# Optimization experiments

Measured on AMD Instinct MI355X. Metric: run time of the kernel, lower is better.

The kernel has to match this reference:

```python
import jax, jax.numpy as jnp
import numpy as np

B, D_IN, D_OUT, N_CTRL = 8192, 512, 512, 8

def setup_inputs() -> dict:
    key = jax.random.key(0)
    k1, k2, k3, k4 = jax.random.split(key, 4)
    inputs = jax.random.normal(k1, (B, D_IN), dtype=jnp.float32)
    # routing weights: positive soft blend coefficients, normalized per sample
    raw = jax.random.uniform(k2, (B, N_CTRL), dtype=jnp.float32)
    weights = raw / jnp.sum(raw, axis=-1, keepdims=True)
    w = jax.random.normal(k3, (N_CTRL, D_IN, D_OUT), dtype=jnp.float32) * 0.05
    b = jax.random.normal(k4, (N_CTRL, D_OUT), dtype=jnp.float32) * 0.05
    return {"inputs": inputs, "weights": weights, "w": w, "b": b}

def reference(inputs, weights, w, b):
    # Original math: w_p = einsum('ji,imk->jmk', weights, w)  [B, D_IN, D_OUT]
    #                out = squeeze(inputs[:, None, :] @ w_p) + weights @ b
    # Fused equivalent avoiding the [B, D_IN, D_OUT] intermediate:
    # run all n_control expert matmuls, then blend by routing weights.
    per_expert = jnp.einsum('bi,cio->cbo', inputs, w)       # [C, B, D_OUT]
    out = jnp.einsum('bc,cbo->bo', weights, per_expert)     # [B, D_OUT]
    out = out + weights @ b                                 # blended bias [B, D_OUT]
    return out
```

## Files before the change

### kernel.cpp

```cpp
#include <hip/hip_runtime.h>

#define B_   8192
#define DIN  512
#define DOUT 512
#define NC   8
#define NCD  (NC * DIN)
#define KSPL 4

typedef float  f32x4 __attribute__((ext_vector_type(4)));
typedef short  s16x8 __attribute__((ext_vector_type(8)));
typedef unsigned short u16x4 __attribute__((ext_vector_type(4)));
typedef unsigned int   u32x4 __attribute__((ext_vector_type(4)));

__device__ __forceinline__ unsigned short f2bf(float f) {
  unsigned u = __builtin_bit_cast(unsigned, f);
  u += 0x7fffu + ((u >> 16) & 1u);
  return (unsigned short)(u >> 16);
}
__device__ __forceinline__ float bf2f(unsigned short h) {
  unsigned u = ((unsigned)h) << 16;
  return __builtin_bit_cast(float, u);
}
__device__ __forceinline__ unsigned cvtpk(float lo, float hi) {
  unsigned r;
  asm("v_cvt_pk_bf16_f32 %0, %1, %2" : "=v"(r) : "v"(lo), "v"(hi));
  return r;
}

__global__ void pack_xw_k(const f32x4* __restrict__ x, u16x4* __restrict__ xb,
                          const float* __restrict__ w, unsigned short* __restrict__ WtF) {
  __shared__ float tile[64][65];
  const int tid = threadIdx.x;
  if (blockIdx.x < 4096) {
    int gid = blockIdx.x * 256 + tid;
    f32x4 v = x[gid];
    u16x4 o;
    o[0] = f2bf(v[0]); o[1] = f2bf(v[1]); o[2] = f2bf(v[2]); o[3] = f2bf(v[3]);
    xb[gid] = o;
    return;
  }
  const int idx = blockIdx.x - 4096;
  const int kb = idx & 63, nb = idx >> 6;
  const int e = kb >> 3, ktl = kb & 7;
#pragma unroll
  for (int it = 0; it < 16; ++it) {
    int u = it * 256 + tid;
    int r = u >> 6, cc = u & 63;
    tile[r][cc] = w[(size_t)(e * 512 + ktl * 64 + r) * DOUT + nb * 64 + cc];
  }
  __syncthreads();
#pragma unroll
  for (int it = 0; it < 2; ++it) {
    int c = it * 256 + tid;
    int n16l = c >> 7, kk = (c >> 6) & 1, l = c & 63;
    int l15 = l & 15, lhi = l >> 4;
    int col_in = n16l * 16 + l15;
    int k_in   = kk * 32 + lhi * 8;
    int n16    = nb * 4 + n16l;
    u16x4 o0, o1;
    o0[0] = f2bf(tile[k_in + 0][col_in]); o0[1] = f2bf(tile[k_in + 1][col_in]);
    o0[2] = f2bf(tile[k_in + 2][col_in]); o0[3] = f2bf(tile[k_in + 3][col_in]);
    o1[0] = f2bf(tile[k_in + 4][col_in]); o1[1] = f2bf(tile[k_in + 5][col_in]);
    o1[2] = f2bf(tile[k_in + 6][col_in]); o1[3] = f2bf(tile[k_in + 7][col_in]);
    size_t base = ((((size_t)e * 32 + n16) * 8 + ktl) * 2 + kk) * 512 + l * 8;
    *(u16x4*)(WtF + base)     = o0;
    *(u16x4*)(WtF + base + 4) = o1;
  }
}

__global__ __launch_bounds__(512, 2) void gemm_k(
    const unsigned short* __restrict__ xb,
    const unsigned short* __restrict__ WtF,
    const float* __restrict__ wt,
    unsigned short* __restrict__ part) {
  extern __shared__ char smem[];
  const int tid  = threadIdx.x;
  const int lane = tid & 63, wid = tid >> 6;
  const int wm = wid >> 2, wn = wid & 3;
  const int l15 = lane & 15, lhi = lane >> 4;

  const int n0   = blockIdx.x;
  const int by   = n0 >> 3;
  const int bx   = (n0 >> 2) & 1;
  const int ks   = n0 & 3;
  const int brow = by * 256, bcol = bx * 256;

  const int srow = tid >> 3, schunk = tid & 7;
  const int swz  = schunk ^ (srow & 7);
  const unsigned short* gA = xb + (size_t)(brow + srow) * DIN + schunk * 8;
  const int adst_off = srow * 128 + swz * 16;

  const unsigned short* bn0 = WtF + (size_t)(ks * 2) * 262144
                                  + (size_t)(bx * 16 + wn * 4 + 0) * 8192 + lane * 8;
  const unsigned short* bn1 = bn0 + 8192;
  const unsigned short* bn2 = bn0 + 16384;
  const unsigned short* bn3 = bn0 + 24576;

  const float* wtp = wt + (size_t)(brow + srow) * NC + ks * 2;
  const float wtv0_0 = wtp[0],            wtv1_0 = wtp[1];
  const float wtv0_1 = wtp[64 * NC],      wtv1_1 = wtp[64 * NC + 1];
  const float wtv0_2 = wtp[128 * NC],     wtv1_2 = wtp[128 * NC + 1];
  const float wtv0_3 = wtp[192 * NC],     wtv1_3 = wtp[192 * NC + 1];

  f32x4 acc[8][4] = {};
  s16x8 areg0, areg1, areg2, areg3;
  s16x8 a[8], b0q[4], b1q[4];
  const int x7    = l15 & 7;
  const int pc0   = (lhi ^ x7) * 16;
  const int pc1   = ((4 + lhi) ^ x7) * 16;
  const int abase = (wm * 128 + l15) * 128;

#define LOAD_B(BQ, et, ktl, kk) {                                            \
    const size_t o_ = (size_t)(et) * 262144 + ((ktl) * 2 + (kk)) * 512;      \
    BQ[0] = *(const s16x8*)(bn0 + o_);                                       \
    BQ[1] = *(const s16x8*)(bn1 + o_);                                       \
    BQ[2] = *(const s16x8*)(bn2 + o_);                                       \
    BQ[3] = *(const s16x8*)(bn3 + o_); }
#define LOAD_AREGS(kt) {                                                     \
    const unsigned short* s_ = gA + ((kt) & 7) * 64;                         \
    areg0 = *(const s16x8*)(s_);                                             \
    areg1 = *(const s16x8*)(s_ + (size_t) 64 * DIN);                         \
    areg2 = *(const s16x8*)(s_ + (size_t)128 * DIN);                         \
    areg3 = *(const s16x8*)(s_ + (size_t)192 * DIN); }
#define SCALE_STORE(AR, S, P, slotb) {                                       \
    u32x4 v_;                                                                \
    v_[0] = cvtpk(bf2f((unsigned short)AR[0]) * (S),                         \
                  bf2f((unsigned short)AR[1]) * (S));                        \
    v_[1] = cvtpk(bf2f((unsigned short)AR[2]) * (S),                         \
                  bf2f((unsigned short)AR[3]) * (S));                        \
    v_[2] = cvtpk(bf2f((unsigned short)AR[4]) * (S),                         \
                  bf2f((unsigned short)AR[5]) * (S));                        \
    v_[3] = cvtpk(bf2f((unsigned short)AR[6]) * (S),                         \
                  bf2f((unsigned short)AR[7]) * (S));                        \
    *(u32x4*)(smem + (slotb) + adst_off + (P) * 8192) = v_; }
#define SCALE_WRITE_ALL(e_, slotb) {                                         \
    SCALE_STORE(areg0, (e_) ? wtv1_0 : wtv0_0, 0, slotb);                    \
    SCALE_STORE(areg1, (e_) ? wtv1_1 : wtv0_1, 1, slotb);                    \
    SCALE_STORE(areg2, (e_) ? wtv1_2 : wtv0_2, 2, slotb);                    \
    SCALE_STORE(areg3, (e_) ? wtv1_3 : wtv0_3, 3, slotb); }
#define RD_A8(slotb, PC) {                                                   \
    const char* pa_ = smem + (slotb) + abase + (PC);                         \
    _Pragma("unroll") for (int m = 0; m < 8; ++m)                            \
      a[m] = *(const s16x8*)(pa_ + m * 2048); }
#define MFMA_HALF(BQ)                                                        \
    _Pragma("unroll") for (int m = 0; m < 8; ++m)                            \
      _Pragma("unroll") for (int n = 0; n < 4; ++n)                          \
        acc[m][n] = __builtin_amdgcn_mfma_f32_16x16x32_bf16(                 \
            a[m], BQ[n], acc[m][n], 0, 0, 0);
#define BAR()   __builtin_amdgcn_s_barrier()
#define PRIO1() __builtin_amdgcn_s_setprio(1)
#define PRIO0() __builtin_amdgcn_s_setprio(0)
#define SBAR0() __builtin_amdgcn_sched_barrier(0)
#define WAITL() asm volatile("s_waitcnt lgkmcnt(0)" ::: "memory")

  LOAD_AREGS(0);
  SCALE_WRITE_ALL(0, 0);
  LOAD_AREGS(1);
  LOAD_B(b0q, 0, 0, 0);
  WAITL();
  BAR();

  for (int t = 0; t < 16; ++t) {
    const int ct = (t & 1) * 32768, ot = 32768 - ct;
    const int ktl = t & 7, et = t >> 3;
    RD_A8(ct, pc0);
    LOAD_B(b1q, et, ktl, 1);
    WAITL(); SBAR0();
    PRIO1(); MFMA_HALF(b0q); PRIO0();
    RD_A8(ct, pc1);
    if (t < 15) {
      SCALE_WRITE_ALL(((t + 1) >> 3), ot);
      if (t < 14) LOAD_AREGS(t + 2);
    }
    WAITL(); SBAR0();
    PRIO1(); MFMA_HALF(b1q); PRIO0();
    if (t < 15) LOAD_B(b0q, ((t + 1) >> 3), ((t + 1) & 7), 0);
    BAR();
  }

  __syncthreads();
  unsigned short* Cs = (unsigned short*)smem;
#pragma unroll
  for (int m = 0; m < 8; ++m)
#pragma unroll
    for (int n = 0; n < 4; ++n) {
      const int row = wm * 128 + m * 16 + lhi * 4;
      const int col = wn * 64 + n * 16 + l15;
      f32x4 v = acc[m][n];
#pragma unroll
      for (int j = 0; j < 4; ++j)
        Cs[(row + j) * 264 + col] = f2bf(v[j]);
    }
  __syncthreads();
  unsigned short* pc = part + (size_t)ks * (B_ * DOUT) + (size_t)brow * DOUT + bcol;
#pragma unroll
  for (int it = 0; it < 16; ++it) {
    const int u = it * 512 + tid;
    const int row = u >> 5, cu = (u & 31) * 8;
    f32x4 v = *(const f32x4*)(Cs + row * 264 + cu);
    *(f32x4*)(pc + (size_t)row * DOUT + cu) = v;
  }
#undef LOAD_B
#undef LOAD_AREGS
#undef SCALE_STORE
#undef SCALE_WRITE_ALL
#undef RD_A8
#undef MFMA_HALF
#undef BAR
#undef PRIO1
#undef PRIO0
#undef SBAR0
#undef WAITL
}

__global__ void reduce_k(const unsigned short* __restrict__ part,
                         const float* __restrict__ wt,
                         const float* __restrict__ bias,
                         float* __restrict__ out) {
  int gid = blockIdx.x * 256 + threadIdx.x;
  int b = gid >> 7;
  int o4 = (gid & 127) << 2;
  float w8[8];
  *(f32x4*)w8       = *(const f32x4*)(wt + (size_t)b * NC);
  *(f32x4*)(w8 + 4) = *(const f32x4*)(wt + (size_t)b * NC + 4);
  f32x4 acc = {0.f, 0.f, 0.f, 0.f};
  const size_t off = (size_t)b * DOUT + o4;
#pragma unroll
  for (int s = 0; s < KSPL; ++s) {
    u16x4 p = *(const u16x4*)(part + (size_t)s * (B_ * DOUT) + off);
#pragma unroll
    for (int i = 0; i < 4; ++i) acc[i] += bf2f(p[i]);
  }
#pragma unroll
  for (int cc = 0; cc < NC; ++cc) {
    f32x4 bi = *(const f32x4*)(bias + cc * DOUT + o4);
#pragma unroll
    for (int i = 0; i < 4; ++i) acc[i] += w8[cc] * bi[i];
  }
  *(f32x4*)(out + off) = acc;
}

__global__ void bias_only_k(const float* __restrict__ wt,
                            const float* __restrict__ bias,
                            float* __restrict__ out) {
  int gid = blockIdx.x * 256 + threadIdx.x;
  int b = gid >> 7;
  int o4 = (gid & 127) << 2;
  float w8[8];
  *(f32x4*)w8       = *(const f32x4*)(wt + (size_t)b * NC);
  *(f32x4*)(w8 + 4) = *(const f32x4*)(wt + (size_t)b * NC + 4);
  f32x4 acc = {0.f, 0.f, 0.f, 0.f};
#pragma unroll
  for (int cc = 0; cc < NC; ++cc) {
    f32x4 bi = *(const f32x4*)(bias + cc * DOUT + o4);
#pragma unroll
    for (int i = 0; i < 4; ++i) acc[i] += w8[cc] * bi[i];
  }
  *(f32x4*)(out + (size_t)b * DOUT + o4) = acc;
}

extern "C" void kernel_launch(void* const* d_in, const int* in_sizes, int n_in,
                              void* d_out, int out_size, void* d_ws, size_t ws_size,
                              hipStream_t stream) {
  const float *x = nullptr, *wtc = nullptr, *w = nullptr, *bias = nullptr;
  for (int i = 0; i < n_in; ++i) {
    switch (in_sizes[i]) {
      case B_ * DIN:        x    = (const float*)d_in[i]; break;
      case B_ * NC:         wtc  = (const float*)d_in[i]; break;
      case NC * DIN * DOUT: w    = (const float*)d_in[i]; break;
      case NC * DOUT:       bias = (const float*)d_in[i]; break;
    }
  }
  float* out = (float*)d_out;

  const size_t XB_ELEMS   = (size_t)B_ * DIN;
  const size_t WT_ELEMS   = (size_t)NC * DIN * DOUT;
  const size_t PART_ELEMS = (size_t)KSPL * B_ * DOUT;
  const size_t need = (XB_ELEMS + WT_ELEMS + PART_ELEMS) * sizeof(unsigned short);

  if (ws_size < need) {
    bias_only_k<<<(B_ * DOUT / 4) / 256, 256, 0, stream>>>(wtc, bias, out);
    return;
  }

  unsigned short* xb   = (unsigned short*)d_ws;
  unsigned short* WtF  = xb + XB_ELEMS;
  unsigned short* part = WtF + WT_ELEMS;

  const int GEMM_LDS = 256 * 264 * 2;
  (void)hipFuncSetAttribute((const void*)gemm_k,
                            hipFuncAttributeMaxDynamicSharedMemorySize, GEMM_LDS);

  pack_xw_k<<<4096 + 512, 256, 0, stream>>>((const f32x4*)x, (u16x4*)xb, w, WtF);
  gemm_k<<<256, 512, GEMM_LDS, stream>>>(xb, WtF, wtc, part);
  reduce_k<<<(B_ * DOUT / 4) / 256, 256, 0, stream>>>(part, wtc, bias, out);
}
```

Before: 62.41 us.

## Shrink GEMM tile to 128x128 with 256 threads and simplify pipeline sync

The fused scale-and-GEMM kernel moves from 256x256 output tiles on 512-thread blocks to 128x128 tiles on 256-thread blocks, launching 1024 blocks instead of 256. LDS use roughly halves, and the explicit lgkmcnt waits, sched barriers and setprio hints are replaced by plain __syncthreads. The aim is more blocks per CU and better latency hiding. In exchange, each tile reuses less data, so A and B traffic from global/L2 rises, and the hand-tuned instruction interleaving is lost.

```diff
diff --git a/kernel.cpp b/kernel.cpp
--- a/kernel.cpp
+++ b/kernel.cpp
@@ -68,7 +68,7 @@
   }
 }
 
-__global__ __launch_bounds__(512, 2) void gemm_k(
+__global__ __launch_bounds__(256) void gemm_k(
     const unsigned short* __restrict__ xb,
     const unsigned short* __restrict__ WtF,
     const float* __restrict__ wt,
@@ -76,14 +76,14 @@
   extern __shared__ char smem[];
   const int tid  = threadIdx.x;
   const int lane = tid & 63, wid = tid >> 6;
-  const int wm = wid >> 2, wn = wid & 3;
+  const int wm = wid >> 1, wn = wid & 1;
   const int l15 = lane & 15, lhi = lane >> 4;
 
   const int n0   = blockIdx.x;
-  const int by   = n0 >> 3;
-  const int bx   = (n0 >> 2) & 1;
   const int ks   = n0 & 3;
-  const int brow = by * 256, bcol = bx * 256;
+  const int bn   = (n0 >> 2) & 3;
+  const int by   = n0 >> 4;
+  const int brow = by * 128, bcol = bn * 128;
 
   const int srow = tid >> 3, schunk = tid & 7;
   const int swz  = schunk ^ (srow & 7);
@@ -91,24 +91,24 @@
   const int adst_off = srow * 128 + swz * 16;
 
   const unsigned short* bn0 = WtF + (size_t)(ks * 2) * 262144
-                                  + (size_t)(bx * 16 + wn * 4 + 0) * 8192 + lane * 8;
+                                  + (size_t)(bn * 8 + wn * 4) * 8192 + lane * 8;
   const unsigned short* bn1 = bn0 + 8192;
   const unsigned short* bn2 = bn0 + 16384;
   const unsigned short* bn3 = bn0 + 24576;
 
   const float* wtp = wt + (size_t)(brow + srow) * NC + ks * 2;
-  const float wtv0_0 = wtp[0],            wtv1_0 = wtp[1];
-  const float wtv0_1 = wtp[64 * NC],      wtv1_1 = wtp[64 * NC + 1];
-  const float wtv0_2 = wtp[128 * NC],     wtv1_2 = wtp[128 * NC + 1];
-  const float wtv0_3 = wtp[192 * NC],     wtv1_3 = wtp[192 * NC + 1];
-
-  f32x4 acc[8][4] = {};
+  const float wtv0_0 = wtp[0],           wtv1_0 = wtp[1];
+  const float wtv0_1 = wtp[32 * NC],     wtv1_1 = wtp[32 * NC + 1];
+  const float wtv0_2 = wtp[64 * NC],     wtv1_2 = wtp[64 * NC + 1];
+  const float wtv0_3 = wtp[96 * NC],     wtv1_3 = wtp[96 * NC + 1];
+
+  f32x4 acc[4][4] = {};
   s16x8 areg0, areg1, areg2, areg3;
-  s16x8 a[8], b0q[4], b1q[4];
+  s16x8 a[4], b0q[4], b1q[4];
   const int x7    = l15 & 7;
   const int pc0   = (lhi ^ x7) * 16;
   const int pc1   = ((4 + lhi) ^ x7) * 16;
-  const int abase = (wm * 128 + l15) * 128;
+  const int abase = (wm * 64 + l15) * 128;
 
 #define LOAD_B(BQ, et, ktl, kk) {                                            \
     const size_t o_ = (size_t)(et) * 262144 + ((ktl) * 2 + (kk)) * 512;      \
@@ -119,9 +119,9 @@
 #define LOAD_AREGS(kt) {                                                     \
     const unsigned short* s_ = gA + ((kt) & 7) * 64;                         \
     areg0 = *(const s16x8*)(s_);                                             \
-    areg1 = *(const s16x8*)(s_ + (size_t) 64 * DIN);                         \
-    areg2 = *(const s16x8*)(s_ + (size_t)128 * DIN);                         \
-    areg3 = *(const s16x8*)(s_ + (size_t)192 * DIN); }
+    areg1 = *(const s16x8*)(s_ + (size_t)32 * DIN);                          \
+    areg2 = *(const s16x8*)(s_ + (size_t)64 * DIN);                          \
+    areg3 = *(const s16x8*)(s_ + (size_t)96 * DIN); }
 #define SCALE_STORE(AR, S, P, slotb) {                                       \
     u32x4 v_;                                                                \
     v_[0] = cvtpk(bf2f((unsigned short)AR[0]) * (S),                         \
@@ -132,85 +132,70 @@
                   bf2f((unsigned short)AR[5]) * (S));                        \
     v_[3] = cvtpk(bf2f((unsigned short)AR[6]) * (S),                         \
                   bf2f((unsigned short)AR[7]) * (S));                        \
-    *(u32x4*)(smem + (slotb) + adst_off + (P) * 8192) = v_; }
+    *(u32x4*)(smem + (slotb) + adst_off + (P) * 4096) = v_; }
 #define SCALE_WRITE_ALL(e_, slotb) {                                         \
     SCALE_STORE(areg0, (e_) ? wtv1_0 : wtv0_0, 0, slotb);                    \
     SCALE_STORE(areg1, (e_) ? wtv1_1 : wtv0_1, 1, slotb);                    \
     SCALE_STORE(areg2, (e_) ? wtv1_2 : wtv0_2, 2, slotb);                    \
     SCALE_STORE(areg3, (e_) ? wtv1_3 : wtv0_3, 3, slotb); }
-#define RD_A8(slotb, PC) {                                                   \
+#define RD_A4(slotb, PC) {                                                   \
     const char* pa_ = smem + (slotb) + abase + (PC);                         \
-    _Pragma("unroll") for (int m = 0; m < 8; ++m)                            \
+    _Pragma("unroll") for (int m = 0; m < 4; ++m)                            \
       a[m] = *(const s16x8*)(pa_ + m * 2048); }
 #define MFMA_HALF(BQ)                                                        \
-    _Pragma("unroll") for (int m = 0; m < 8; ++m)                            \
+    _Pragma("unroll") for (int m = 0; m < 4; ++m)                            \
       _Pragma("unroll") for (int n = 0; n < 4; ++n)                          \
         acc[m][n] = __builtin_amdgcn_mfma_f32_16x16x32_bf16(                 \
             a[m], BQ[n], acc[m][n], 0, 0, 0);
-#define BAR()   __builtin_amdgcn_s_barrier()
-#define PRIO1() __builtin_amdgcn_s_setprio(1)
-#define PRIO0() __builtin_amdgcn_s_setprio(0)
-#define SBAR0() __builtin_amdgcn_sched_barrier(0)
-#define WAITL() asm volatile("s_waitcnt lgkmcnt(0)" ::: "memory")
 
   LOAD_AREGS(0);
   SCALE_WRITE_ALL(0, 0);
   LOAD_AREGS(1);
   LOAD_B(b0q, 0, 0, 0);
-  WAITL();
-  BAR();
+  __syncthreads();
 
   for (int t = 0; t < 16; ++t) {
-    const int ct = (t & 1) * 32768, ot = 32768 - ct;
-    const int ktl = t & 7, et = t >> 3;
-    RD_A8(ct, pc0);
-    LOAD_B(b1q, et, ktl, 1);
-    WAITL(); SBAR0();
-    PRIO1(); MFMA_HALF(b0q); PRIO0();
-    RD_A8(ct, pc1);
+    const int ct = (t & 1) * 16384, ot = 16384 - ct;
+    RD_A4(ct, pc0);
+    LOAD_B(b1q, (t >> 3), (t & 7), 1);
+    MFMA_HALF(b0q);
     if (t < 15) {
       SCALE_WRITE_ALL(((t + 1) >> 3), ot);
       if (t < 14) LOAD_AREGS(t + 2);
     }
-    WAITL(); SBAR0();
-    PRIO1(); MFMA_HALF(b1q); PRIO0();
+    RD_A4(ct, pc1);
+    MFMA_HALF(b1q);
     if (t < 15) LOAD_B(b0q, ((t + 1) >> 3), ((t + 1) & 7), 0);
-    BAR();
-  }
-
-  __syncthreads();
+    __syncthreads();
+  }
+
   unsigned short* Cs = (unsigned short*)smem;
 #pragma unroll
-  for (int m = 0; m < 8; ++m)
+  for (int m = 0; m < 4; ++m)
 #pragma unroll
     for (int n = 0; n < 4; ++n) {
-      const int row = wm * 128 + m * 16 + lhi * 4;
+      const int row = wm * 64 + m * 16 + lhi * 4;
       const int col = wn * 64 + n * 16 + l15;
       f32x4 v = acc[m][n];
 #pragma unroll
       for (int j = 0; j < 4; ++j)
-        Cs[(row + j) * 264 + col] = f2bf(v[j]);
+        Cs[(row + j) * 132 + col] = f2bf(v[j]);
     }
   __syncthreads();
   unsigned short* pc = part + (size_t)ks * (B_ * DOUT) + (size_t)brow * DOUT + bcol;
 #pragma unroll
-  for (int it = 0; it < 16; ++it) {
-    const int u = it * 512 + tid;
-    const int row = u >> 5, cu = (u & 31) * 8;
-    f32x4 v = *(const f32x4*)(Cs + row * 264 + cu);
+  for (int it = 0; it < 8; ++it) {
+    const int u = it * 256 + tid;
+    const int row = u >> 4, cu = (u & 15) * 8;
+    f32x4 v = *(const f32x4*)(Cs + row * 132 + cu);
     *(f32x4*)(pc + (size_t)row * DOUT + cu) = v;
   }
 #undef LOAD_B
 #undef LOAD_AREGS
 #undef SCALE_STORE
 #undef SCALE_WRITE_ALL
-#undef RD_A8
+#undef RD_A4
 #undef MFMA_HALF
-#undef BAR
-#undef PRIO1
-#undef PRIO0
-#undef SBAR0
-#undef WAITL
 }
 
 __global__ void reduce_k(const unsigned short* __restrict__ part,
@@ -287,11 +272,11 @@
   unsigned short* WtF  = xb + XB_ELEMS;
   unsigned short* part = WtF + WT_ELEMS;
 
-  const int GEMM_LDS = 256 * 264 * 2;
+  const int GEMM_LDS = 128 * 132 * 2;
   (void)hipFuncSetAttribute((const void*)gemm_k,
                             hipFuncAttributeMaxDynamicSharedMemorySize, GEMM_LDS);
 
   pack_xw_k<<<4096 + 512, 256, 0, stream>>>((const f32x4*)x, (u16x4*)xb, w, WtF);
-  gemm_k<<<256, 512, GEMM_LDS, stream>>>(xb, WtF, wtc, part);
+  gemm_k<<<1024, 256, GEMM_LDS, stream>>>(xb, WtF, wtc, part);
   reduce_k<<<(B_ * DOUT / 4) / 256, 256, 0, stream>>>(part, wtc, bias, out);
 }
```

New measurement: 75.04 us. 20.2% more time.
